# Performance work log

Measured on AMD Instinct MI355X. Metric: run time of the kernel, lower is better.

The kernel has to match this reference:

```python
import jax, jax.numpy as jnp
import numpy as np

N = 50000   # nodes
E = 800000  # edges
F = 128     # num_features
H = 128     # n_hidden_channels
C = 16      # num_classes


def _gcn_conv(x, W, b, src, dst, dinv):
    """PyG GCNConv: h = x @ W; out = D^-1/2 (A+I) D^-1/2 h + b."""
    h = x @ W                                   # [N, out]
    coef = dinv[src] * dinv[dst]                # [E]
    msg = h[src] * coef[:, None]                # gather + scale
    agg = jax.ops.segment_sum(msg, dst, num_segments=N)
    agg = agg + h * (dinv * dinv)[:, None]      # self-loop term
    return agg + b


def setup_inputs() -> dict:
    key = jax.random.key(0)
    ks = jax.random.split(key, 8)
    x = jax.random.normal(ks[0], (N, F), dtype=jnp.float32)
    edge_index = jax.random.randint(ks[1], (2, E), 0, N, dtype=jnp.int64)

    def glorot(k, fan_in, fan_out):
        return jax.random.normal(k, (fan_in, fan_out), dtype=jnp.float32) / np.sqrt(fan_in)

    return {
        "x": x,
        "edge_index": edge_index,
        "W1": glorot(ks[2], F, H), "b1": jnp.zeros((H,), jnp.float32),
        "W2": glorot(ks[3], H, H), "b2": jnp.zeros((H,), jnp.float32),
        "W3": glorot(ks[4], H, H), "b3": jnp.zeros((H,), jnp.float32),
        "W4": glorot(ks[5], H, C), "b4": jnp.zeros((C,), jnp.float32),
        "Wc": glorot(ks[6], C, 1), "bc": jnp.zeros((1,), jnp.float32),
    }


def reference(x, edge_index, W1, b1, W2, b2, W3, b3, W4, b4, Wc, bc):
    src, dst = edge_index[0], edge_index[1]
    # degree with self-loops (edge_weight = 1)
    deg = jax.ops.segment_sum(jnp.ones((E,), x.dtype), dst, num_segments=N) + 1.0
    dinv = jax.lax.rsqrt(deg)

    out = _gcn_conv(x, W1, b1, src, dst, dinv)
    out = jnp.tanh(_gcn_conv(out, W2, b2, src, dst, dinv))
    out = jax.nn.leaky_relu(_gcn_conv(out, W3, b3, src, dst, dinv), negative_slope=0.01)
    out = jax.nn.leaky_relu(_gcn_conv(out, W4, b4, src, dst, dinv), negative_slope=0.01)
    out = jax.nn.elu(out @ Wc + bc)             # [N, 1]
    return out
```

## Files before the change

### kernel.cpp

```cpp
#include <hip/hip_runtime.h>
#include <hip/hip_bf16.h>
#include <cstdint>
#include <cstddef>

#define NN 50000
#define NE 800000

using short8v = __attribute__((ext_vector_type(8))) short;
using f32x4 = __attribute__((ext_vector_type(4))) float;

__device__ __forceinline__ unsigned short f2bf(float f) {
    unsigned u = __float_as_uint(f);
    u += 0x7fffu + ((u >> 16) & 1u);
    return (unsigned short)(u >> 16);
}
__device__ __forceinline__ float bf2f(unsigned s) {
    return __uint_as_float(s << 16);
}


__global__ __launch_bounds__(256) void zero_i32(int* __restrict__ p, int n) {
    int i = blockIdx.x * 256 + threadIdx.x;
    if (i < n) p[i] = 0;
}

__global__ __launch_bounds__(256) void count_deg(const int* __restrict__ dst,
                                                 int* __restrict__ cnt, int E) {
    int e = blockIdx.x * 256 + threadIdx.x;
    if (e < E) atomicAdd(&cnt[dst[e]], 1);
}

__global__ __launch_bounds__(1024) void scan1(const int* __restrict__ cnt,
                                              int* __restrict__ local,
                                              int* __restrict__ bsum,
                                              float* __restrict__ dinv, int N) {
    int t = threadIdx.x;
    int g = blockIdx.x * 1024 + t;
    int lane = t & 63, w = t >> 6;
    int v = (g < N) ? cnt[g] : 0;
    if (g < N) dinv[g] = rsqrtf((float)v + 1.0f);
    int x = v;
    #pragma unroll
    for (int off = 1; off < 64; off <<= 1) {
        int y = __shfl_up(x, off);
        if (lane >= off) x += y;
    }
    __shared__ int wsum[16];
    if (lane == 63) wsum[w] = x;
    __syncthreads();
    if (t < 16) {
        int s = wsum[t];
        int xx = s;
        #pragma unroll
        for (int off = 1; off < 16; off <<= 1) {
            int y = __shfl_up(xx, off);
            if (t >= off) xx += y;
        }
        wsum[t] = xx - s;
    }
    __syncthreads();
    int excl = wsum[w] + x - v;
    if (g < N) local[g] = excl;
    if (t == 1023) bsum[blockIdx.x] = excl + v;
}

__global__ __launch_bounds__(64) void scan2(int* __restrict__ bsum, int NB) {
    int t = threadIdx.x;
    int v = (t < NB) ? bsum[t] : 0;
    int x = v;
    #pragma unroll
    for (int off = 1; off < 64; off <<= 1) {
        int y = __shfl_up(x, off);
        if (t >= off) x += y;
    }
    if (t < NB) bsum[t] = x - v;
}

__global__ __launch_bounds__(256) void scan3(const int* __restrict__ local,
                                             const int* __restrict__ bsum,
                                             int* __restrict__ rowptr,
                                             int* __restrict__ cursor, int N, int E) {
    int g = blockIdx.x * 256 + threadIdx.x;
    if (g < N) {
        int r = local[g] + bsum[g >> 10];
        rowptr[g] = r;
        cursor[g] = r;
    }
    if (g == 0) rowptr[N] = E;
}

__global__ __launch_bounds__(256) void scatter_csr(const int* __restrict__ src,
                                                   const int* __restrict__ dst,
                                                   int* __restrict__ cursor,
                                                   int* __restrict__ csr, int E) {
    int e = blockIdx.x * 256 + threadIdx.x;
    if (e < E) {
        int d = dst[e];
        int pos = atomicAdd(&cursor[d], 1);
        csr[pos] = src[e];
    }
}


__global__ __launch_bounds__(256) void cvt_split(const float* __restrict__ X,
                                                 unsigned* __restrict__ Xh,
                                                 unsigned* __restrict__ Xl,
                                                 int total4) {
    int i = blockIdx.x * 256 + threadIdx.x;
    int stride = gridDim.x * 256;
    for (; i < total4; i += stride) {
        float4 v = ((const float4*)X)[i];
        unsigned short h0 = f2bf(v.x), h1 = f2bf(v.y), h2 = f2bf(v.z), h3 = f2bf(v.w);
        float l0 = v.x - bf2f(h0), l1 = v.y - bf2f(h1);
        float l2 = v.z - bf2f(h2), l3 = v.w - bf2f(h3);
        uint2 hh = make_uint2((unsigned)h0 | ((unsigned)h1 << 16),
                              (unsigned)h2 | ((unsigned)h3 << 16));
        uint2 ll = make_uint2((unsigned)f2bf(l0) | ((unsigned)f2bf(l1) << 16),
                              (unsigned)f2bf(l2) | ((unsigned)f2bf(l3) << 16));
        ((uint2*)Xh)[i] = hh;
        ((uint2*)Xl)[i] = ll;
    }
}


__global__ __launch_bounds__(256) void gemm_mfma(const unsigned* __restrict__ Xh,
                                                 const unsigned* __restrict__ Xl,
                                                 const float* __restrict__ W,
                                                 const float* __restrict__ dinv,
                                                 float* __restrict__ out, int N) {
    __shared__ unsigned short xh[64 * 128];
    __shared__ unsigned short xl[64 * 128];
    __shared__ unsigned short wh[128 * 40];
    __shared__ unsigned short wl[128 * 40];
    int tid = threadIdx.x;
    int lane = tid & 63, wv = tid >> 6;
    int row0 = blockIdx.x * 64;

    #pragma unroll
    for (int i = 0; i < 4; ++i) {
        int id = i * 256 + tid;
        int r = id >> 4, kc = id & 15;
        uint4 vh = make_uint4(0, 0, 0, 0), vl = make_uint4(0, 0, 0, 0);
        if (row0 + r < N) {
            vh = *(const uint4*)&Xh[(size_t)(row0 + r) * 64 + kc * 4];
            vl = *(const uint4*)&Xl[(size_t)(row0 + r) * 64 + kc * 4];
        }
        int off = r * 128 + ((kc * 8) ^ ((r & 7) << 3));
        *(uint4*)&xh[off] = vh;
        *(uint4*)&xl[off] = vl;
    }

    int mstrip = (wv & 1) * 32;
    int nbase = (wv >> 1) * 64;
    f32x4 acc[2][4] = {};

    for (int ks = 0; ks < 4; ++ks) {
        __syncthreads();
        #pragma unroll
        for (int i = 0; i < 8; ++i) {
            int id = i * 256 + tid;
            int kp = id >> 7, n = id & 127;
            int k0 = ks * 32 + kp * 2;
            float a = W[k0 * 128 + n];
            float b = W[(k0 + 1) * 128 + n];
            unsigned short ah = f2bf(a), bh = f2bf(b);
            float alo = a - bf2f(ah), blo = b - bf2f(bh);
            *(unsigned*)&wh[n * 40 + kp * 2] = (unsigned)ah | ((unsigned)bh << 16);
            *(unsigned*)&wl[n * 40 + kp * 2] =
                (unsigned)f2bf(alo) | ((unsigned)f2bf(blo) << 16);
        }
        __syncthreads();

        short8v afh[2], afl[2];
        #pragma unroll
        for (int mt = 0; mt < 2; ++mt) {
            int r = mstrip + mt * 16 + (lane & 15);
            int off = r * 128 + ((ks * 32 + ((lane >> 4) * 8)) ^ ((r & 7) << 3));
            afh[mt] = *(const short8v*)&xh[off];
            afl[mt] = *(const short8v*)&xl[off];
        }
        #pragma unroll
        for (int nt = 0; nt < 4; ++nt) {
            int c = nbase + nt * 16 + (lane & 15);
            int boff = c * 40 + (lane >> 4) * 8;
            short8v bfh = *(const short8v*)&wh[boff];
            short8v bfl = *(const short8v*)&wl[boff];
            #pragma unroll
            for (int mt = 0; mt < 2; ++mt) {
                acc[mt][nt] = __builtin_amdgcn_mfma_f32_16x16x32_bf16(afh[mt], bfh, acc[mt][nt], 0, 0, 0);
                acc[mt][nt] = __builtin_amdgcn_mfma_f32_16x16x32_bf16(afh[mt], bfl, acc[mt][nt], 0, 0, 0);
                acc[mt][nt] = __builtin_amdgcn_mfma_f32_16x16x32_bf16(afl[mt], bfh, acc[mt][nt], 0, 0, 0);
            }
        }
    }

    #pragma unroll
    for (int mt = 0; mt < 2; ++mt) {
        #pragma unroll
        for (int i = 0; i < 4; ++i) {
            int r = row0 + mstrip + mt * 16 + (lane >> 4) * 4 + i;
            if (r < N) {
                float dv = dinv[r];
                #pragma unroll
                for (int nt = 0; nt < 4; ++nt) {
                    int cg = nbase + nt * 16 + (lane & 15);
                    out[(size_t)r * 128 + cg] = acc[mt][nt][i] * dv;
                }
            }
        }
    }
}

__global__ __launch_bounds__(256) void gemm16(const unsigned* __restrict__ Xh,
                                              const unsigned* __restrict__ Xl,
                                              const float* __restrict__ W,
                                              const float* __restrict__ dinv,
                                              float* __restrict__ out, int N) {
    __shared__ float xs[64][128];
    __shared__ float ws4[128][16];
    int tid = threadIdx.x;
    int row0 = blockIdx.x * 64;

    #pragma unroll
    for (int i = 0; i < 2; ++i)
        ((float4*)ws4)[i * 256 + tid] = ((const float4*)W)[i * 256 + tid];

    #pragma unroll
    for (int i = 0; i < 8; ++i) {
        int id = i * 256 + tid;
        int r = id >> 5, c4 = id & 31;
        float4 v = make_float4(0.f, 0.f, 0.f, 0.f);
        if (row0 + r < N) {
            uint2 hh = *(const uint2*)&Xh[(size_t)(row0 + r) * 64 + c4 * 2];
            uint2 ll = *(const uint2*)&Xl[(size_t)(row0 + r) * 64 + c4 * 2];
            v.x = bf2f(hh.x & 0xffffu) + bf2f(ll.x & 0xffffu);
            v.y = bf2f(hh.x >> 16) + bf2f(ll.x >> 16);
            v.z = bf2f(hh.y & 0xffffu) + bf2f(ll.y & 0xffffu);
            v.w = bf2f(hh.y >> 16) + bf2f(ll.y >> 16);
        }
        *(float4*)&xs[r][c4 * 4] = v;
    }
    __syncthreads();

    int ty = tid >> 4, tx = tid & 15;
    float acc[4] = {};
    #pragma unroll 4
    for (int k = 0; k < 128; ++k) {
        float wvv = ws4[k][tx];
        #pragma unroll
        for (int i = 0; i < 4; ++i)
            acc[i] = fmaf(xs[ty * 4 + i][k], wvv, acc[i]);
    }
    #pragma unroll
    for (int i = 0; i < 4; ++i) {
        int r = row0 + ty * 4 + i;
        if (r < N) out[(size_t)r * 16 + tx] = acc[i] * dinv[r];
    }
}


template <int ACT>
__global__ __launch_bounds__(256) void agg128(const float* __restrict__ HS,
                                              const int* __restrict__ rp,
                                              const int* __restrict__ csr,
                                              const float* __restrict__ dinv,
                                              const float* __restrict__ b,
                                              unsigned* __restrict__ Xh,
                                              unsigned* __restrict__ Xl, int N) {
    int wid = threadIdx.x >> 6, lane = threadIdx.x & 63;
    int n = blockIdx.x * 4 + wid;
    if (n >= N) return;
    const float2* H2 = (const float2*)HS;
    float2 a0 = H2[(size_t)n * 64 + lane];
    float2 a1 = make_float2(0.f, 0.f), a2 = a1, a3 = a1;
    float2 a4 = a1, a5 = a1, a6 = a1, a7 = a1;
    int e = rp[n], end = rp[n + 1];
    for (; e + 8 <= end; e += 8) {
        int s0 = csr[e], s1 = csr[e + 1], s2 = csr[e + 2], s3 = csr[e + 3];
        int s4 = csr[e + 4], s5 = csr[e + 5], s6 = csr[e + 6], s7 = csr[e + 7];
        float2 v0 = H2[(size_t)s0 * 64 + lane];
        float2 v1 = H2[(size_t)s1 * 64 + lane];
        float2 v2 = H2[(size_t)s2 * 64 + lane];
        float2 v3 = H2[(size_t)s3 * 64 + lane];
        float2 v4 = H2[(size_t)s4 * 64 + lane];
        float2 v5 = H2[(size_t)s5 * 64 + lane];
        float2 v6 = H2[(size_t)s6 * 64 + lane];
        float2 v7 = H2[(size_t)s7 * 64 + lane];
        a0.x += v0.x; a0.y += v0.y; a1.x += v1.x; a1.y += v1.y;
        a2.x += v2.x; a2.y += v2.y; a3.x += v3.x; a3.y += v3.y;
        a4.x += v4.x; a4.y += v4.y; a5.x += v5.x; a5.y += v5.y;
        a6.x += v6.x; a6.y += v6.y; a7.x += v7.x; a7.y += v7.y;
    }
    if (e + 4 <= end) {
        int s0 = csr[e], s1 = csr[e + 1], s2 = csr[e + 2], s3 = csr[e + 3];
        float2 v0 = H2[(size_t)s0 * 64 + lane];
        float2 v1 = H2[(size_t)s1 * 64 + lane];
        float2 v2 = H2[(size_t)s2 * 64 + lane];
        float2 v3 = H2[(size_t)s3 * 64 + lane];
        a4.x += v0.x; a4.y += v0.y; a5.x += v1.x; a5.y += v1.y;
        a6.x += v2.x; a6.y += v2.y; a7.x += v3.x; a7.y += v3.y;
        e += 4;
    }
    for (; e < end; ++e) {
        int s = csr[e];
        float2 v = H2[(size_t)s * 64 + lane];
        a0.x += v.x; a0.y += v.y;
    }
    float accx = ((a0.x + a1.x) + (a2.x + a3.x)) + ((a4.x + a5.x) + (a6.x + a7.x));
    float accy = ((a0.y + a1.y) + (a2.y + a3.y)) + ((a4.y + a5.y) + (a6.y + a7.y));
    float dv = dinv[n];
    float2 bb = ((const float2*)b)[lane];
    float ox = fmaf(dv, accx, bb.x);
    float oy = fmaf(dv, accy, bb.y);
    if (ACT == 1) { ox = tanhf(ox); oy = tanhf(oy); }
    else if (ACT == 2) {
        ox = ox > 0.f ? ox : 0.01f * ox;
        oy = oy > 0.f ? oy : 0.01f * oy;
    }
    unsigned short h0 = f2bf(ox), h1 = f2bf(oy);
    float l0 = ox - bf2f(h0), l1 = oy - bf2f(h1);
    Xh[(size_t)n * 64 + lane] = (unsigned)h0 | ((unsigned)h1 << 16);
    Xl[(size_t)n * 64 + lane] = (unsigned)f2bf(l0) | ((unsigned)f2bf(l1) << 16);
}


__global__ __launch_bounds__(256) void final_layer(const float* __restrict__ HS4,
                                                   const int* __restrict__ rp,
                                                   const int* __restrict__ csr,
                                                   const float* __restrict__ dinv,
                                                   const float* __restrict__ b4,
                                                   const float* __restrict__ Wc,
                                                   const float* __restrict__ bc,
                                                   float* __restrict__ out, int N) {
    int wid = threadIdx.x >> 6, lane = threadIdx.x & 63;
    int n = blockIdx.x * 4 + wid;
    if (n >= N) return;
    int f = lane & 15, g = lane >> 4;
    float acc = 0.f;
    int beg = rp[n], end = rp[n + 1];
    for (int e = beg + g; e < end; e += 4)
        acc += HS4[(size_t)csr[e] * 16 + f];
    acc += __shfl_xor(acc, 16);
    acc += __shfl_xor(acc, 32);
    acc += HS4[(size_t)n * 16 + f];
    float t = fmaf(dinv[n], acc, b4[f]);
    t = t > 0.f ? t : 0.01f * t;
    float p = t * Wc[f];
    p += __shfl_xor(p, 1);
    p += __shfl_xor(p, 2);
    p += __shfl_xor(p, 4);
    p += __shfl_xor(p, 8);
    if (lane == 0) {
        float z = p + bc[0];
        out[n] = z > 0.f ? z : expm1f(z);
    }
}


extern "C" void kernel_launch(void* const* d_in, const int* in_sizes, int n_in,
                              void* d_out, int out_size, void* d_ws, size_t ws_size,
                              hipStream_t stream) {
    const int N = NN, E = NE;
    const float* x  = (const float*)d_in[0];
    const int*   ei = (const int*)d_in[1];
    const float* W1 = (const float*)d_in[2];
    const float* b1 = (const float*)d_in[3];
    const float* W2 = (const float*)d_in[4];
    const float* b2 = (const float*)d_in[5];
    const float* W3 = (const float*)d_in[6];
    const float* b3 = (const float*)d_in[7];
    const float* W4 = (const float*)d_in[8];
    const float* b4 = (const float*)d_in[9];
    const float* Wc = (const float*)d_in[10];
    const float* bc = (const float*)d_in[11];
    float* out = (float*)d_out;
    const int* src = ei;
    const int* dst = ei + E;

    char* p = (char*)d_ws;
    auto carve = [&](size_t bytes) -> char* {
        char* q = p;
        p += (bytes + 255) & ~(size_t)255;
        return q;
    };
    int*      cnt    = (int*)carve((size_t)N * 4);
    int*      rowptr = (int*)carve((size_t)(N + 1) * 4);
    int*      cursor = (int*)carve((size_t)N * 4);
    float*    dinv   = (float*)carve((size_t)N * 4);
    int*      csr    = (int*)carve((size_t)E * 4);
    int*      locsc  = (int*)carve((size_t)N * 4);
    int*      bsum   = (int*)carve((size_t)64 * 4);
    unsigned* Xh     = (unsigned*)carve((size_t)N * 64 * 4);
    unsigned* Xl     = (unsigned*)carve((size_t)N * 64 * 4);
    float*    bufB   = (float*)carve((size_t)N * 128 * 4);

    const int NB = (N + 1023) / 1024;

    zero_i32<<<(N + 255) / 256, 256, 0, stream>>>(cnt, N);
    count_deg<<<(E + 255) / 256, 256, 0, stream>>>(dst, cnt, E);
    scan1<<<NB, 1024, 0, stream>>>(cnt, locsc, bsum, dinv, N);
    scan2<<<1, 64, 0, stream>>>(bsum, NB);
    scan3<<<(N + 255) / 256, 256, 0, stream>>>(locsc, bsum, rowptr, cursor, N, E);
    scatter_csr<<<(E + 255) / 256, 256, 0, stream>>>(src, dst, cursor, csr, E);

    int gblocks = (N + 63) / 64;
    int ablocks = (N + 3) / 4;

    cvt_split<<<2048, 256, 0, stream>>>(x, Xh, Xl, N * 128 / 4);

    gemm_mfma<<<gblocks, 256, 0, stream>>>(Xh, Xl, W1, dinv, bufB, N);
    agg128<0><<<ablocks, 256, 0, stream>>>(bufB, rowptr, csr, dinv, b1, Xh, Xl, N);
    gemm_mfma<<<gblocks, 256, 0, stream>>>(Xh, Xl, W2, dinv, bufB, N);
    agg128<1><<<ablocks, 256, 0, stream>>>(bufB, rowptr, csr, dinv, b2, Xh, Xl, N);
    gemm_mfma<<<gblocks, 256, 0, stream>>>(Xh, Xl, W3, dinv, bufB, N);
    agg128<2><<<ablocks, 256, 0, stream>>>(bufB, rowptr, csr, dinv, b3, Xh, Xl, N);
    gemm16<<<gblocks, 256, 0, stream>>>(Xh, Xl, W4, dinv, bufB, N);
    final_layer<<<ablocks, 256, 0, stream>>>(bufB, rowptr, csr, dinv, b4, Wc, bc, out, N);
}
```

Before: 393.4 us.

## Record edge ranks during degree count and widen aggregation gather unroll

The degree-count pass now stores each edge's atomic return value as its rank within its destination row. The CSR scatter then writes to rowptr[d]+rank[e] with no second atomic pass. Per-node counters are padded to a 17-int stride to spread atomic contention across cache lines. Separately, the aggregation loop is unrolled to 16 neighbor gathers in flight. The costs are a 17x larger counter array to zero and read with strided access, an extra rank array, and higher register pressure in agg128.

```diff
diff --git a/kernel.cpp b/kernel.cpp
--- a/kernel.cpp
+++ b/kernel.cpp
@@ -24,20 +24,24 @@
     if (i < n) p[i] = 0;
 }
 
-__global__ __launch_bounds__(256) void count_deg(const int* __restrict__ dst,
-                                                 int* __restrict__ cnt, int E) {
+__global__ __launch_bounds__(256) void count_deg_rank(const int* __restrict__ dst,
+                                                      int* __restrict__ cntP,
+                                                      int* __restrict__ rank, int E) {
     int e = blockIdx.x * 256 + threadIdx.x;
-    if (e < E) atomicAdd(&cnt[dst[e]], 1);
-}
-
-__global__ __launch_bounds__(1024) void scan1(const int* __restrict__ cnt,
+    if (e < E) {
+        int d = dst[e];
+        rank[e] = atomicAdd(&cntP[d * 17], 1);
+    }
+}
+
+__global__ __launch_bounds__(1024) void scan1(const int* __restrict__ cntP,
                                               int* __restrict__ local,
                                               int* __restrict__ bsum,
                                               float* __restrict__ dinv, int N) {
     int t = threadIdx.x;
     int g = blockIdx.x * 1024 + t;
     int lane = t & 63, w = t >> 6;
-    int v = (g < N) ? cnt[g] : 0;
+    int v = (g < N) ? cntP[g * 17] : 0;
     if (g < N) dinv[g] = rsqrtf((float)v + 1.0f);
     int x = v;
     #pragma unroll
@@ -78,26 +82,21 @@
 
 __global__ __launch_bounds__(256) void scan3(const int* __restrict__ local,
                                              const int* __restrict__ bsum,
-                                             int* __restrict__ rowptr,
-                                             int* __restrict__ cursor, int N, int E) {
+                                             int* __restrict__ rowptr, int N, int E) {
     int g = blockIdx.x * 256 + threadIdx.x;
-    if (g < N) {
-        int r = local[g] + bsum[g >> 10];
-        rowptr[g] = r;
-        cursor[g] = r;
-    }
+    if (g < N) rowptr[g] = local[g] + bsum[g >> 10];
     if (g == 0) rowptr[N] = E;
 }
 
-__global__ __launch_bounds__(256) void scatter_csr(const int* __restrict__ src,
-                                                   const int* __restrict__ dst,
-                                                   int* __restrict__ cursor,
-                                                   int* __restrict__ csr, int E) {
+__global__ __launch_bounds__(256) void scatter_plain(const int* __restrict__ src,
+                                                     const int* __restrict__ dst,
+                                                     const int* __restrict__ rowptr,
+                                                     const int* __restrict__ rank,
+                                                     int* __restrict__ csr, int E) {
     int e = blockIdx.x * 256 + threadIdx.x;
     if (e < E) {
         int d = dst[e];
-        int pos = atomicAdd(&cursor[d], 1);
-        csr[pos] = src[e];
+        csr[rowptr[d] + rank[e]] = src[e];
     }
 }
 
@@ -271,43 +270,62 @@
     int n = blockIdx.x * 4 + wid;
     if (n >= N) return;
     const float2* H2 = (const float2*)HS;
-    float2 a0 = H2[(size_t)n * 64 + lane];
-    float2 a1 = make_float2(0.f, 0.f), a2 = a1, a3 = a1;
-    float2 a4 = a1, a5 = a1, a6 = a1, a7 = a1;
+    float2 acc[8];
+    acc[0] = H2[(size_t)n * 64 + lane];
+    #pragma unroll
+    for (int j = 1; j < 8; ++j) acc[j] = make_float2(0.f, 0.f);
     int e = rp[n], end = rp[n + 1];
-    for (; e + 8 <= end; e += 8) {
-        int s0 = csr[e], s1 = csr[e + 1], s2 = csr[e + 2], s3 = csr[e + 3];
-        int s4 = csr[e + 4], s5 = csr[e + 5], s6 = csr[e + 6], s7 = csr[e + 7];
-        float2 v0 = H2[(size_t)s0 * 64 + lane];
-        float2 v1 = H2[(size_t)s1 * 64 + lane];
-        float2 v2 = H2[(size_t)s2 * 64 + lane];
-        float2 v3 = H2[(size_t)s3 * 64 + lane];
-        float2 v4 = H2[(size_t)s4 * 64 + lane];
-        float2 v5 = H2[(size_t)s5 * 64 + lane];
-        float2 v6 = H2[(size_t)s6 * 64 + lane];
-        float2 v7 = H2[(size_t)s7 * 64 + lane];
-        a0.x += v0.x; a0.y += v0.y; a1.x += v1.x; a1.y += v1.y;
-        a2.x += v2.x; a2.y += v2.y; a3.x += v3.x; a3.y += v3.y;
-        a4.x += v4.x; a4.y += v4.y; a5.x += v5.x; a5.y += v5.y;
-        a6.x += v6.x; a6.y += v6.y; a7.x += v7.x; a7.y += v7.y;
+    for (; e + 16 <= end; e += 16) {
+        int s[16];
+        #pragma unroll
+        for (int j = 0; j < 16; ++j) s[j] = csr[e + j];
+        float2 v[16];
+        #pragma unroll
+        for (int j = 0; j < 16; ++j) v[j] = H2[(size_t)s[j] * 64 + lane];
+        #pragma unroll
+        for (int j = 0; j < 8; ++j) {
+            acc[j].x += v[j].x + v[j + 8].x;
+            acc[j].y += v[j].y + v[j + 8].y;
+        }
+    }
+    if (e + 8 <= end) {
+        int s[8];
+        #pragma unroll
+        for (int j = 0; j < 8; ++j) s[j] = csr[e + j];
+        float2 v[8];
+        #pragma unroll
+        for (int j = 0; j < 8; ++j) v[j] = H2[(size_t)s[j] * 64 + lane];
+        #pragma unroll
+        for (int j = 0; j < 8; ++j) {
+            acc[j].x += v[j].x;
+            acc[j].y += v[j].y;
+        }
+        e += 8;
     }
     if (e + 4 <= end) {
-        int s0 = csr[e], s1 = csr[e + 1], s2 = csr[e + 2], s3 = csr[e + 3];
-        float2 v0 = H2[(size_t)s0 * 64 + lane];
-        float2 v1 = H2[(size_t)s1 * 64 + lane];
-        float2 v2 = H2[(size_t)s2 * 64 + lane];
-        float2 v3 = H2[(size_t)s3 * 64 + lane];
-        a4.x += v0.x; a4.y += v0.y; a5.x += v1.x; a5.y += v1.y;
-        a6.x += v2.x; a6.y += v2.y; a7.x += v3.x; a7.y += v3.y;
+        int s[4];
+        #pragma unroll
+        for (int j = 0; j < 4; ++j) s[j] = csr[e + j];
+        float2 v[4];
+        #pragma unroll
+        for (int j = 0; j < 4; ++j) v[j] = H2[(size_t)s[j] * 64 + lane];
+        #pragma unroll
+        for (int j = 0; j < 4; ++j) {
+            acc[j + 4].x += v[j].x;
+            acc[j + 4].y += v[j].y;
+        }
         e += 4;
     }
     for (; e < end; ++e) {
         int s = csr[e];
         float2 v = H2[(size_t)s * 64 + lane];
-        a0.x += v.x; a0.y += v.y;
-    }
-    float accx = ((a0.x + a1.x) + (a2.x + a3.x)) + ((a4.x + a5.x) + (a6.x + a7.x));
-    float accy = ((a0.y + a1.y) + (a2.y + a3.y)) + ((a4.y + a5.y) + (a6.y + a7.y));
+        acc[0].x += v.x;
+        acc[0].y += v.y;
+    }
+    float accx = ((acc[0].x + acc[1].x) + (acc[2].x + acc[3].x)) +
+                 ((acc[4].x + acc[5].x) + (acc[6].x + acc[7].x));
+    float accy = ((acc[0].y + acc[1].y) + (acc[2].y + acc[3].y)) +
+                 ((acc[4].y + acc[5].y) + (acc[6].y + acc[7].y));
     float dv = dinv[n];
     float2 bb = ((const float2*)b)[lane];
     float ox = fmaf(dv, accx, bb.x);
@@ -383,9 +401,9 @@
         p += (bytes + 255) & ~(size_t)255;
         return q;
     };
-    int*      cnt    = (int*)carve((size_t)N * 4);
+    int*      cntP   = (int*)carve((size_t)N * 17 * 4);
+    int*      rank   = (int*)carve((size_t)E * 4);
     int*      rowptr = (int*)carve((size_t)(N + 1) * 4);
-    int*      cursor = (int*)carve((size_t)N * 4);
     float*    dinv   = (float*)carve((size_t)N * 4);
     int*      csr    = (int*)carve((size_t)E * 4);
     int*      locsc  = (int*)carve((size_t)N * 4);
@@ -396,12 +414,12 @@
 
     const int NB = (N + 1023) / 1024;
 
-    zero_i32<<<(N + 255) / 256, 256, 0, stream>>>(cnt, N);
-    count_deg<<<(E + 255) / 256, 256, 0, stream>>>(dst, cnt, E);
-    scan1<<<NB, 1024, 0, stream>>>(cnt, locsc, bsum, dinv, N);
+    zero_i32<<<(N * 17 + 255) / 256, 256, 0, stream>>>(cntP, N * 17);
+    count_deg_rank<<<(E + 255) / 256, 256, 0, stream>>>(dst, cntP, rank, E);
+    scan1<<<NB, 1024, 0, stream>>>(cntP, locsc, bsum, dinv, N);
     scan2<<<1, 64, 0, stream>>>(bsum, NB);
-    scan3<<<(N + 255) / 256, 256, 0, stream>>>(locsc, bsum, rowptr, cursor, N, E);
-    scatter_csr<<<(E + 255) / 256, 256, 0, stream>>>(src, dst, cursor, csr, E);
+    scan3<<<(N + 255) / 256, 256, 0, stream>>>(locsc, bsum, rowptr, N, E);
+    scatter_plain<<<(E + 255) / 256, 256, 0, stream>>>(src, dst, rowptr, rank, csr, E);
 
     int gblocks = (N + 63) / 64;
     int ablocks = (N + 3) / 4;
```

Result: faster. 357.1 us (-9.2%).

## Fuse input split into GEMM, pre-split weights once, rank-based CSR build

Applied to the files above, without the earlier changes.

Degree counting now also records each edge's rank inside its destination row, using a counter array padded to 64 bytes per node to reduce atomic contention. The CSR scatter then writes to rowptr+rank with no second atomic pass, and the cursor array is dropped. A single small kernel pre-transposes and splits W1-W3 into bf16 hi/lo, so the GEMM reads B fragments straight from global memory and no longer converts weights in LDS with per-k-step barriers. The first GEMM converts fp32 x to hi/lo inline, which removes the separate cvt_split pass over x. The trade-offs are a larger zeroing pass, an extra rank array, and uncached global loads for B fragments.

```diff
diff --git a/kernel.cpp b/kernel.cpp
--- a/kernel.cpp
+++ b/kernel.cpp
@@ -24,20 +24,24 @@
     if (i < n) p[i] = 0;
 }
 
-__global__ __launch_bounds__(256) void count_deg(const int* __restrict__ dst,
-                                                 int* __restrict__ cnt, int E) {
+__global__ __launch_bounds__(256) void count_deg_rank(const int* __restrict__ dst,
+                                                      int* __restrict__ cntP,
+                                                      int* __restrict__ rank, int E) {
     int e = blockIdx.x * 256 + threadIdx.x;
-    if (e < E) atomicAdd(&cnt[dst[e]], 1);
-}
-
-__global__ __launch_bounds__(1024) void scan1(const int* __restrict__ cnt,
+    if (e < E) {
+        int d = dst[e];
+        rank[e] = atomicAdd(&cntP[d << 4], 1);
+    }
+}
+
+__global__ __launch_bounds__(1024) void scan1(const int* __restrict__ cntP,
                                               int* __restrict__ local,
                                               int* __restrict__ bsum,
                                               float* __restrict__ dinv, int N) {
     int t = threadIdx.x;
     int g = blockIdx.x * 1024 + t;
     int lane = t & 63, w = t >> 6;
-    int v = (g < N) ? cnt[g] : 0;
+    int v = (g < N) ? cntP[g << 4] : 0;
     if (g < N) dinv[g] = rsqrtf((float)v + 1.0f);
     int x = v;
     #pragma unroll
@@ -78,60 +82,51 @@
 
 __global__ __launch_bounds__(256) void scan3(const int* __restrict__ local,
                                              const int* __restrict__ bsum,
-                                             int* __restrict__ rowptr,
-                                             int* __restrict__ cursor, int N, int E) {
+                                             int* __restrict__ rowptr, int N, int E) {
     int g = blockIdx.x * 256 + threadIdx.x;
-    if (g < N) {
-        int r = local[g] + bsum[g >> 10];
-        rowptr[g] = r;
-        cursor[g] = r;
-    }
+    if (g < N) rowptr[g] = local[g] + bsum[g >> 10];
     if (g == 0) rowptr[N] = E;
 }
 
-__global__ __launch_bounds__(256) void scatter_csr(const int* __restrict__ src,
-                                                   const int* __restrict__ dst,
-                                                   int* __restrict__ cursor,
-                                                   int* __restrict__ csr, int E) {
+__global__ __launch_bounds__(256) void scatter_plain(const int* __restrict__ src,
+                                                     const int* __restrict__ dst,
+                                                     const int* __restrict__ rowptr,
+                                                     const int* __restrict__ rank,
+                                                     int* __restrict__ csr, int E) {
     int e = blockIdx.x * 256 + threadIdx.x;
     if (e < E) {
         int d = dst[e];
-        int pos = atomicAdd(&cursor[d], 1);
-        csr[pos] = src[e];
-    }
-}
-
-
-__global__ __launch_bounds__(256) void cvt_split(const float* __restrict__ X,
-                                                 unsigned* __restrict__ Xh,
-                                                 unsigned* __restrict__ Xl,
-                                                 int total4) {
+        csr[rowptr[d] + rank[e]] = src[e];
+    }
+}
+
+
+__global__ __launch_bounds__(256) void split_wt(const float* __restrict__ Wa,
+                                                const float* __restrict__ Wb,
+                                                const float* __restrict__ Wc,
+                                                unsigned short* __restrict__ WTh,
+                                                unsigned short* __restrict__ WTl) {
+    const float* W = (blockIdx.y == 0) ? Wa : (blockIdx.y == 1) ? Wb : Wc;
     int i = blockIdx.x * 256 + threadIdx.x;
-    int stride = gridDim.x * 256;
-    for (; i < total4; i += stride) {
-        float4 v = ((const float4*)X)[i];
-        unsigned short h0 = f2bf(v.x), h1 = f2bf(v.y), h2 = f2bf(v.z), h3 = f2bf(v.w);
-        float l0 = v.x - bf2f(h0), l1 = v.y - bf2f(h1);
-        float l2 = v.z - bf2f(h2), l3 = v.w - bf2f(h3);
-        uint2 hh = make_uint2((unsigned)h0 | ((unsigned)h1 << 16),
-                              (unsigned)h2 | ((unsigned)h3 << 16));
-        uint2 ll = make_uint2((unsigned)f2bf(l0) | ((unsigned)f2bf(l1) << 16),
-                              (unsigned)f2bf(l2) | ((unsigned)f2bf(l3) << 16));
-        ((uint2*)Xh)[i] = hh;
-        ((uint2*)Xl)[i] = ll;
-    }
-}
-
-
-__global__ __launch_bounds__(256) void gemm_mfma(const unsigned* __restrict__ Xh,
-                                                 const unsigned* __restrict__ Xl,
-                                                 const float* __restrict__ W,
+    int n = i >> 7, k = i & 127;
+    float v = W[k * 128 + n];
+    unsigned short h = f2bf(v);
+    float lo = v - bf2f(h);
+    size_t base = (size_t)blockIdx.y * 16384 + i;
+    WTh[base] = h;
+    WTl[base] = f2bf(lo);
+}
+
+
+template <bool F32IN>
+__global__ __launch_bounds__(256) void gemm_mfma(const void* __restrict__ Xin,
+                                                 const void* __restrict__ Xlin,
+                                                 const unsigned short* __restrict__ WTh,
+                                                 const unsigned short* __restrict__ WTl,
                                                  const float* __restrict__ dinv,
                                                  float* __restrict__ out, int N) {
     __shared__ unsigned short xh[64 * 128];
     __shared__ unsigned short xl[64 * 128];
-    __shared__ unsigned short wh[128 * 40];
-    __shared__ unsigned short wl[128 * 40];
     int tid = threadIdx.x;
     int lane = tid & 63, wv = tid >> 6;
     int row0 = blockIdx.x * 64;
@@ -142,35 +137,37 @@
         int r = id >> 4, kc = id & 15;
         uint4 vh = make_uint4(0, 0, 0, 0), vl = make_uint4(0, 0, 0, 0);
         if (row0 + r < N) {
-            vh = *(const uint4*)&Xh[(size_t)(row0 + r) * 64 + kc * 4];
-            vl = *(const uint4*)&Xl[(size_t)(row0 + r) * 64 + kc * 4];
+            if constexpr (F32IN) {
+                const float* Xf = (const float*)Xin;
+                float4 a = *(const float4*)(Xf + (size_t)(row0 + r) * 128 + kc * 8);
+                float4 b = *(const float4*)(Xf + (size_t)(row0 + r) * 128 + kc * 8 + 4);
+                unsigned short h0 = f2bf(a.x), h1 = f2bf(a.y), h2 = f2bf(a.z), h3 = f2bf(a.w);
+                unsigned short h4 = f2bf(b.x), h5 = f2bf(b.y), h6 = f2bf(b.z), h7 = f2bf(b.w);
+                vh = make_uint4((unsigned)h0 | ((unsigned)h1 << 16),
+                                (unsigned)h2 | ((unsigned)h3 << 16),
+                                (unsigned)h4 | ((unsigned)h5 << 16),
+                                (unsigned)h6 | ((unsigned)h7 << 16));
+                vl = make_uint4((unsigned)f2bf(a.x - bf2f(h0)) | ((unsigned)f2bf(a.y - bf2f(h1)) << 16),
+                                (unsigned)f2bf(a.z - bf2f(h2)) | ((unsigned)f2bf(a.w - bf2f(h3)) << 16),
+                                (unsigned)f2bf(b.x - bf2f(h4)) | ((unsigned)f2bf(b.y - bf2f(h5)) << 16),
+                                (unsigned)f2bf(b.z - bf2f(h6)) | ((unsigned)f2bf(b.w - bf2f(h7)) << 16));
+            } else {
+                vh = *(const uint4*)&((const unsigned*)Xin)[(size_t)(row0 + r) * 64 + kc * 4];
+                vl = *(const uint4*)&((const unsigned*)Xlin)[(size_t)(row0 + r) * 64 + kc * 4];
+            }
         }
         int off = r * 128 + ((kc * 8) ^ ((r & 7) << 3));
         *(uint4*)&xh[off] = vh;
         *(uint4*)&xl[off] = vl;
     }
+    __syncthreads();
 
     int mstrip = (wv & 1) * 32;
     int nbase = (wv >> 1) * 64;
     f32x4 acc[2][4] = {};
 
+    #pragma unroll
     for (int ks = 0; ks < 4; ++ks) {
-        __syncthreads();
-        #pragma unroll
-        for (int i = 0; i < 8; ++i) {
-            int id = i * 256 + tid;
-            int kp = id >> 7, n = id & 127;
-            int k0 = ks * 32 + kp * 2;
-            float a = W[k0 * 128 + n];
-            float b = W[(k0 + 1) * 128 + n];
-            unsigned short ah = f2bf(a), bh = f2bf(b);
-            float alo = a - bf2f(ah), blo = b - bf2f(bh);
-            *(unsigned*)&wh[n * 40 + kp * 2] = (unsigned)ah | ((unsigned)bh << 16);
-            *(unsigned*)&wl[n * 40 + kp * 2] =
-                (unsigned)f2bf(alo) | ((unsigned)f2bf(blo) << 16);
-        }
-        __syncthreads();
-
         short8v afh[2], afl[2];
         #pragma unroll
         for (int mt = 0; mt < 2; ++mt) {
@@ -182,9 +179,9 @@
         #pragma unroll
         for (int nt = 0; nt < 4; ++nt) {
             int c = nbase + nt * 16 + (lane & 15);
-            int boff = c * 40 + (lane >> 4) * 8;
-            short8v bfh = *(const short8v*)&wh[boff];
-            short8v bfl = *(const short8v*)&wl[boff];
+            size_t goff = (size_t)c * 128 + ks * 32 + (lane >> 4) * 8;
+            short8v bfh = *(const short8v*)&WTh[goff];
+            short8v bfl = *(const short8v*)&WTl[goff];
             #pragma unroll
             for (int mt = 0; mt < 2; ++mt) {
                 acc[mt][nt] = __builtin_amdgcn_mfma_f32_16x16x32_bf16(afh[mt], bfh, acc[mt][nt], 0, 0, 0);
@@ -383,36 +380,37 @@
         p += (bytes + 255) & ~(size_t)255;
         return q;
     };
-    int*      cnt    = (int*)carve((size_t)N * 4);
-    int*      rowptr = (int*)carve((size_t)(N + 1) * 4);
-    int*      cursor = (int*)carve((size_t)N * 4);
-    float*    dinv   = (float*)carve((size_t)N * 4);
-    int*      csr    = (int*)carve((size_t)E * 4);
-    int*      locsc  = (int*)carve((size_t)N * 4);
-    int*      bsum   = (int*)carve((size_t)64 * 4);
-    unsigned* Xh     = (unsigned*)carve((size_t)N * 64 * 4);
-    unsigned* Xl     = (unsigned*)carve((size_t)N * 64 * 4);
-    float*    bufB   = (float*)carve((size_t)N * 128 * 4);
+    int*            cntP   = (int*)carve((size_t)N * 16 * 4);
+    int*            rank   = (int*)carve((size_t)E * 4);
+    int*            rowptr = (int*)carve((size_t)(N + 1) * 4);
+    float*          dinv   = (float*)carve((size_t)N * 4);
+    int*            csr    = (int*)carve((size_t)E * 4);
+    int*            locsc  = (int*)carve((size_t)N * 4);
+    int*            bsum   = (int*)carve((size_t)64 * 4);
+    unsigned short* WTh    = (unsigned short*)carve((size_t)3 * 16384 * 2);
+    unsigned short* WTl    = (unsigned short*)carve((size_t)3 * 16384 * 2);
+    unsigned*       Xh     = (unsigned*)carve((size_t)N * 64 * 4);
+    unsigned*       Xl     = (unsigned*)carve((size_t)N * 64 * 4);
+    float*          bufB   = (float*)carve((size_t)N * 128 * 4);
 
     const int NB = (N + 1023) / 1024;
 
-    zero_i32<<<(N + 255) / 256, 256, 0, stream>>>(cnt, N);
-    count_deg<<<(E + 255) / 256, 256, 0, stream>>>(dst, cnt, E);
-    scan1<<<NB, 1024, 0, stream>>>(cnt, locsc, bsum, dinv, N);
+    zero_i32<<<(N * 16 + 255) / 256, 256, 0, stream>>>(cntP, N * 16);
+    count_deg_rank<<<(E + 255) / 256, 256, 0, stream>>>(dst, cntP, rank, E);
+    scan1<<<NB, 1024, 0, stream>>>(cntP, locsc, bsum, dinv, N);
     scan2<<<1, 64, 0, stream>>>(bsum, NB);
-    scan3<<<(N + 255) / 256, 256, 0, stream>>>(locsc, bsum, rowptr, cursor, N, E);
-    scatter_csr<<<(E + 255) / 256, 256, 0, stream>>>(src, dst, cursor, csr, E);
+    scan3<<<(N + 255) / 256, 256, 0, stream>>>(locsc, bsum, rowptr, N, E);
+    scatter_plain<<<(E + 255) / 256, 256, 0, stream>>>(src, dst, rowptr, rank, csr, E);
+    split_wt<<<dim3(64, 3), 256, 0, stream>>>(W1, W2, W3, WTh, WTl);
 
     int gblocks = (N + 63) / 64;
     int ablocks = (N + 3) / 4;
 
-    cvt_split<<<2048, 256, 0, stream>>>(x, Xh, Xl, N * 128 / 4);
-
-    gemm_mfma<<<gblocks, 256, 0, stream>>>(Xh, Xl, W1, dinv, bufB, N);
+    gemm_mfma<true><<<gblocks, 256, 0, stream>>>(x, nullptr, WTh, WTl, dinv, bufB, N);
     agg128<0><<<ablocks, 256, 0, stream>>>(bufB, rowptr, csr, dinv, b1, Xh, Xl, N);
-    gemm_mfma<<<gblocks, 256, 0, stream>>>(Xh, Xl, W2, dinv, bufB, N);
+    gemm_mfma<false><<<gblocks, 256, 0, stream>>>(Xh, Xl, WTh + 16384, WTl + 16384, dinv, bufB, N);
     agg128<1><<<ablocks, 256, 0, stream>>>(bufB, rowptr, csr, dinv, b2, Xh, Xl, N);
-    gemm_mfma<<<gblocks, 256, 0, stream>>>(Xh, Xl, W3, dinv, bufB, N);
+    gemm_mfma<false><<<gblocks, 256, 0, stream>>>(Xh, Xl, WTh + 32768, WTl + 32768, dinv, bufB, N);
     agg128<2><<<ablocks, 256, 0, stream>>>(bufB, rowptr, csr, dinv, b3, Xh, Xl, N);
     gemm16<<<gblocks, 256, 0, stream>>>(Xh, Xl, W4, dinv, bufB, N);
     final_layer<<<ablocks, 256, 0, stream>>>(bufB, rowptr, csr, dinv, b4, Wc, bc, out, N);
```

Measured after the change: 348.7 us. 11.4% less time.
